# Optimization experiments

Hardware: AMD Instinct MI355X
Metric: run time of the kernel (lower is better)

The kernel has to match this reference:

```python
import jax, jax.numpy as jnp
import numpy as np

N = 100000      # nodes
E = 1200000     # edges
F = 16          # in_cont_dim
EMB = 8         # emb_dim
H = 64          # hidden_dim
NL = 3          # num_layers
NT = 32         # num_func_types


def setup_inputs() -> dict:
    key = jax.random.key(0)
    ks = jax.random.split(key, 10)
    s = lambda k, sh: jax.random.normal(k, sh, jnp.float32) * 0.05
    inp = {}
    inp["x_cont"] = jax.random.normal(ks[0], (N, F), jnp.float32)
    inp["func_type"] = jax.random.randint(ks[1], (N,), 0, NT)
    inp["edge_index"] = jax.random.randint(ks[2], (2, E), 0, N)
    inp["emb_table"] = s(ks[3], (NT, EMB))
    inp["W_in"] = s(ks[4], (F + EMB, H)); inp["b_in"] = jnp.zeros((H,), jnp.float32)
    inp["W_g"] = s(ks[5], (NL, H, H));    inp["b_g"] = jnp.zeros((NL, H), jnp.float32)
    inp["W_o1"] = s(ks[6], (H, H));       inp["b_o1"] = jnp.zeros((H,), jnp.float32)
    inp["W_o2"] = s(ks[7], (H, 1));       inp["b_o2"] = jnp.zeros((1,), jnp.float32)
    return inp


def _gcn_layer(x, src, dst, deg_isq, W, b):
    # PyG GCNConv: h = x W; out_i = sum_{j->i} d_i^-1/2 d_j^-1/2 h_j + d_i^-1 h_i + b
    h = x @ W                                   # [N, H]
    norm = deg_isq[src] * deg_isq[dst]          # [E]
    agg = jax.ops.segment_sum(norm[:, None] * h[src], dst, num_segments=N)
    agg = agg + (deg_isq * deg_isq)[:, None] * h  # self-loop contribution
    return agg + b


def reference(x_cont, func_type, edge_index, emb_table, W_in, b_in,
              W_g, b_g, W_o1, b_o1, W_o2, b_o2):
    src, dst = edge_index[0], edge_index[1]
    # degree with self loops (weight 1), computed at target nodes as in gcn_norm
    deg = 1.0 + jax.ops.segment_sum(jnp.ones((E,), x_cont.dtype), dst, num_segments=N)
    deg_isq = jax.lax.rsqrt(deg)
    x = jnp.concatenate([x_cont, emb_table[func_type]], axis=-1)  # [N, F+EMB]
    x = jax.nn.relu(x @ W_in + b_in)
    for i in range(NL):
        x = jax.nn.relu(_gcn_layer(x, src, dst, deg_isq, W_g[i], b_g[i]))
        # dropout is identity in eval mode
    h = jax.nn.relu(x @ W_o1 + b_o1)
    return (h @ W_o2 + b_o2)[:, 0]  # [N]
```

## Files before the change

kernel.cpp:

```cpp
#include <hip/hip_runtime.h>

#define HD 64
#define FC 16
#define FEMB 8

__global__ void k_count_rank(const int* __restrict__ dst, int* __restrict__ cnt,
                             int* __restrict__ rank, int E) {
    int e = blockIdx.x * blockDim.x + threadIdx.x;
    if (e >= E) return;
    rank[e] = atomicAdd(&cnt[dst[e]], 1);
}

__global__ void k_scan1(const int* __restrict__ cnt, int* __restrict__ row_part,
                        int* __restrict__ bsum, float* __restrict__ disq, int n) {
    __shared__ int s[256];
    int t = threadIdx.x;
    int i = blockIdx.x * 256 + t;
    int v = (i < n) ? cnt[i] : 0;
    if (i < n) disq[i] = rsqrtf(1.0f + (float)v);
    s[t] = v;
    __syncthreads();
    for (int off = 1; off < 256; off <<= 1) {
        int a = (t >= off) ? s[t - off] : 0;
        __syncthreads();
        s[t] += a;
        __syncthreads();
    }
    if (i < n) row_part[i] = s[t] - v;
    if (t == 255) bsum[blockIdx.x] = s[255];
}

__global__ void k_scan2(int* __restrict__ bsum, int nb) {
    __shared__ int s[1024];
    int t = threadIdx.x;
    int v = (t < nb) ? bsum[t] : 0;
    s[t] = v;
    __syncthreads();
    for (int off = 1; off < 1024; off <<= 1) {
        int a = (t >= off) ? s[t - off] : 0;
        __syncthreads();
        s[t] += a;
        __syncthreads();
    }
    if (t < nb) bsum[t] = s[t] - v;
}

__global__ void k_scan3(int* __restrict__ row_part, const int* __restrict__ bsum, int n) {
    int stride = gridDim.x * blockDim.x;
    for (int i = blockIdx.x * blockDim.x + threadIdx.x; i < n; i += stride)
        row_part[i] += bsum[i >> 8];
}

__global__ void k_reorder(const int* __restrict__ src, const int* __restrict__ dst,
                          const int* __restrict__ rank, const int* __restrict__ rowst,
                          int* __restrict__ csr, int E) {
    int e = blockIdx.x * blockDim.x + threadIdx.x;
    if (e >= E) return;
    csr[rowst[dst[e]] + rank[e]] = src[e];
}

__global__ void k_input(const float* __restrict__ xc, const int* __restrict__ ft,
                        const float* __restrict__ emb, const float* __restrict__ Win,
                        const float* __restrict__ bin, const float* __restrict__ disq,
                        float* __restrict__ y, int n) {
    int lane = threadIdx.x & 63;
    int wid  = (blockIdx.x * blockDim.x + threadIdx.x) >> 6;
    if (wid >= n) return;
    float acc = bin[lane];
    const float* xr = xc + (size_t)wid * FC;
#pragma unroll
    for (int k = 0; k < FC; k++)
        acc = fmaf(xr[k], Win[k * HD + lane], acc);
    int t = ft[wid];
    const float* er = emb + (size_t)t * FEMB;
#pragma unroll
    for (int k = 0; k < FEMB; k++)
        acc = fmaf(er[k], Win[(FC + k) * HD + lane], acc);
    y[(size_t)wid * HD + lane] = fmaxf(acc, 0.0f) * disq[wid];
}

__global__ void k_agg(const float4* __restrict__ y4, const int* __restrict__ csr,
                      const int* __restrict__ rs, const int* __restrict__ deg,
                      const float* __restrict__ disq, float4* __restrict__ agg4, int n) {
    int lane = threadIdx.x & 63;
    int node = (blockIdx.x * blockDim.x + threadIdx.x) >> 6;
    if (node >= n) return;
    int g  = lane >> 4;
    int c4 = lane & 15;
    int start = rs[node];
    int end   = start + deg[node];
    float4 acc = {0, 0, 0, 0};
    for (int j = start; j < end; j += 16) {
#pragma unroll
        for (int slot = 0; slot < 4; slot++) {
            int e = j + slot * 4 + g;
            bool ok = e < end;
            int ec = ok ? e : j;
            int s = csr[ec];
            float4 v = y4[(size_t)s * 16 + c4];
            if (ok) {
                acc.x += v.x; acc.y += v.y; acc.z += v.z; acc.w += v.w;
            }
        }
    }
    acc.x += __shfl_xor(acc.x, 16); acc.y += __shfl_xor(acc.y, 16);
    acc.z += __shfl_xor(acc.z, 16); acc.w += __shfl_xor(acc.w, 16);
    acc.x += __shfl_xor(acc.x, 32); acc.y += __shfl_xor(acc.y, 32);
    acc.z += __shfl_xor(acc.z, 32); acc.w += __shfl_xor(acc.w, 32);
    if (g == 0) {
        float4 self = y4[(size_t)node * 16 + c4];
        float di = disq[node];
        float4 o;
        o.x = di * (acc.x + self.x);
        o.y = di * (acc.y + self.y);
        o.z = di * (acc.z + self.z);
        o.w = di * (acc.w + self.w);
        agg4[(size_t)node * 16 + c4] = o;
    }
}

__global__ __launch_bounds__(256, 4)
void k_mm(float* __restrict__ x, const float* __restrict__ W,
          const float* __restrict__ b, const float* __restrict__ disq, int n) {
    __shared__ float4 ws4[64][16];
    __shared__ float4 xs4[64][17];
    int tid = threadIdx.x;
    int node0 = blockIdx.x * 64;

    for (int i = tid; i < 1024; i += 256)
        ws4[i >> 4][i & 15] = ((const float4*)W)[i];
    for (int i = tid; i < 1024; i += 256) {
        int nn = i >> 4, k4 = i & 15;
        int row = node0 + nn; if (row >= n) row = n - 1;
        xs4[nn][k4] = ((const float4*)(x + (size_t)row * HD))[k4];
    }
    __syncthreads();

    int tc4 = tid & 15;
    int tn  = (tid >> 4) * 4;
    float4 ac0 = {0,0,0,0}, ac1 = {0,0,0,0}, ac2 = {0,0,0,0}, ac3 = {0,0,0,0};

#pragma unroll 4
    for (int k4 = 0; k4 < 16; k4++) {
        float4 w0 = ws4[k4 * 4 + 0][tc4];
        float4 w1 = ws4[k4 * 4 + 1][tc4];
        float4 w2 = ws4[k4 * 4 + 2][tc4];
        float4 w3 = ws4[k4 * 4 + 3][tc4];
#pragma unroll
        for (int i = 0; i < 4; i++) {
            float4 xv = xs4[tn + i][k4];
            float4* ac = (i == 0) ? &ac0 : (i == 1) ? &ac1 : (i == 2) ? &ac2 : &ac3;
            ac->x = fmaf(xv.x, w0.x, ac->x); ac->y = fmaf(xv.x, w0.y, ac->y);
            ac->z = fmaf(xv.x, w0.z, ac->z); ac->w = fmaf(xv.x, w0.w, ac->w);
            ac->x = fmaf(xv.y, w1.x, ac->x); ac->y = fmaf(xv.y, w1.y, ac->y);
            ac->z = fmaf(xv.y, w1.z, ac->z); ac->w = fmaf(xv.y, w1.w, ac->w);
            ac->x = fmaf(xv.z, w2.x, ac->x); ac->y = fmaf(xv.z, w2.y, ac->y);
            ac->z = fmaf(xv.z, w2.z, ac->z); ac->w = fmaf(xv.z, w2.w, ac->w);
            ac->x = fmaf(xv.w, w3.x, ac->x); ac->y = fmaf(xv.w, w3.y, ac->y);
            ac->z = fmaf(xv.w, w3.z, ac->z); ac->w = fmaf(xv.w, w3.w, ac->w);
        }
    }

    float4 bb = ((const float4*)b)[tc4];
    float4 accs[4] = {ac0, ac1, ac2, ac3};
#pragma unroll
    for (int i = 0; i < 4; i++) {
        int row = node0 + tn + i;
        if (row < n) {
            float dq = disq[row];
            float4 o;
            o.x = fmaxf(accs[i].x + bb.x, 0.0f) * dq;
            o.y = fmaxf(accs[i].y + bb.y, 0.0f) * dq;
            o.z = fmaxf(accs[i].z + bb.z, 0.0f) * dq;
            o.w = fmaxf(accs[i].w + bb.w, 0.0f) * dq;
            *(float4*)(x + (size_t)row * HD + tc4 * 4) = o;
        }
    }
}

__global__ __launch_bounds__(256, 4)
void k_mm_head(const float* __restrict__ x, const float* __restrict__ W,
               const float* __restrict__ b, const float* __restrict__ W1,
               const float* __restrict__ b1, const float* __restrict__ W2,
               const float* __restrict__ b2, float* __restrict__ out, int n) {
    __shared__ float4 ws4[64][16];
    __shared__ float4 xs4[64][17];
    int tid = threadIdx.x;
    int node0 = blockIdx.x * 64;

    for (int i = tid; i < 1024; i += 256)
        ws4[i >> 4][i & 15] = ((const float4*)W)[i];
    for (int i = tid; i < 1024; i += 256) {
        int nn = i >> 4, k4 = i & 15;
        int row = node0 + nn; if (row >= n) row = n - 1;
        xs4[nn][k4] = ((const float4*)(x + (size_t)row * HD))[k4];
    }
    __syncthreads();

    int tc4 = tid & 15;
    int tn  = (tid >> 4) * 4;

    float4 ac0 = {0,0,0,0}, ac1 = {0,0,0,0}, ac2 = {0,0,0,0}, ac3 = {0,0,0,0};
#pragma unroll 4
    for (int k4 = 0; k4 < 16; k4++) {
        float4 w0 = ws4[k4 * 4 + 0][tc4];
        float4 w1 = ws4[k4 * 4 + 1][tc4];
        float4 w2 = ws4[k4 * 4 + 2][tc4];
        float4 w3 = ws4[k4 * 4 + 3][tc4];
#pragma unroll
        for (int i = 0; i < 4; i++) {
            float4 xv = xs4[tn + i][k4];
            float4* ac = (i == 0) ? &ac0 : (i == 1) ? &ac1 : (i == 2) ? &ac2 : &ac3;
            ac->x = fmaf(xv.x, w0.x, ac->x); ac->y = fmaf(xv.x, w0.y, ac->y);
            ac->z = fmaf(xv.x, w0.z, ac->z); ac->w = fmaf(xv.x, w0.w, ac->w);
            ac->x = fmaf(xv.y, w1.x, ac->x); ac->y = fmaf(xv.y, w1.y, ac->y);
            ac->z = fmaf(xv.y, w1.z, ac->z); ac->w = fmaf(xv.y, w1.w, ac->w);
            ac->x = fmaf(xv.z, w2.x, ac->x); ac->y = fmaf(xv.z, w2.y, ac->y);
            ac->z = fmaf(xv.z, w2.z, ac->z); ac->w = fmaf(xv.z, w2.w, ac->w);
            ac->x = fmaf(xv.w, w3.x, ac->x); ac->y = fmaf(xv.w, w3.y, ac->y);
            ac->z = fmaf(xv.w, w3.z, ac->z); ac->w = fmaf(xv.w, w3.w, ac->w);
        }
    }
    __syncthreads();

    {
        float4 bb = ((const float4*)b)[tc4];
        float4 accs[4] = {ac0, ac1, ac2, ac3};
#pragma unroll
        for (int i = 0; i < 4; i++) {
            float4 o;
            o.x = fmaxf(accs[i].x + bb.x, 0.0f);
            o.y = fmaxf(accs[i].y + bb.y, 0.0f);
            o.z = fmaxf(accs[i].z + bb.z, 0.0f);
            o.w = fmaxf(accs[i].w + bb.w, 0.0f);
            xs4[tn + i][tc4] = o;
        }
    }
    for (int i = tid; i < 1024; i += 256)
        ws4[i >> 4][i & 15] = ((const float4*)W1)[i];
    __syncthreads();

    float4 bc0 = {0,0,0,0}, bc1 = {0,0,0,0}, bc2 = {0,0,0,0}, bc3 = {0,0,0,0};
#pragma unroll 4
    for (int k4 = 0; k4 < 16; k4++) {
        float4 w0 = ws4[k4 * 4 + 0][tc4];
        float4 w1 = ws4[k4 * 4 + 1][tc4];
        float4 w2 = ws4[k4 * 4 + 2][tc4];
        float4 w3 = ws4[k4 * 4 + 3][tc4];
#pragma unroll
        for (int i = 0; i < 4; i++) {
            float4 xv = xs4[tn + i][k4];
            float4* ac = (i == 0) ? &bc0 : (i == 1) ? &bc1 : (i == 2) ? &bc2 : &bc3;
            ac->x = fmaf(xv.x, w0.x, ac->x); ac->y = fmaf(xv.x, w0.y, ac->y);
            ac->z = fmaf(xv.x, w0.z, ac->z); ac->w = fmaf(xv.x, w0.w, ac->w);
            ac->x = fmaf(xv.y, w1.x, ac->x); ac->y = fmaf(xv.y, w1.y, ac->y);
            ac->z = fmaf(xv.y, w1.z, ac->z); ac->w = fmaf(xv.y, w1.w, ac->w);
            ac->x = fmaf(xv.z, w2.x, ac->x); ac->y = fmaf(xv.z, w2.y, ac->y);
            ac->z = fmaf(xv.z, w2.z, ac->z); ac->w = fmaf(xv.z, w2.w, ac->w);
            ac->x = fmaf(xv.w, w3.x, ac->x); ac->y = fmaf(xv.w, w3.y, ac->y);
            ac->z = fmaf(xv.w, w3.z, ac->z); ac->w = fmaf(xv.w, w3.w, ac->w);
        }
    }

    float4 b1v = ((const float4*)b1)[tc4];
    float4 w2v = ((const float4*)W2)[tc4];
    float b2v  = b2[0];
    float4 bcs[4] = {bc0, bc1, bc2, bc3};
#pragma unroll
    for (int i = 0; i < 4; i++) {
        float s = fmaxf(bcs[i].x + b1v.x, 0.0f) * w2v.x
                + fmaxf(bcs[i].y + b1v.y, 0.0f) * w2v.y
                + fmaxf(bcs[i].z + b1v.z, 0.0f) * w2v.z
                + fmaxf(bcs[i].w + b1v.w, 0.0f) * w2v.w;
        s += __shfl_xor(s, 1);
        s += __shfl_xor(s, 2);
        s += __shfl_xor(s, 4);
        s += __shfl_xor(s, 8);
        int row = node0 + tn + i;
        if (tc4 == 0 && row < n) out[row] = s + b2v;
    }
}

extern "C" void kernel_launch(void* const* d_in, const int* in_sizes, int n_in,
                              void* d_out, int out_size, void* d_ws, size_t ws_size,
                              hipStream_t stream) {
    const float* x_cont = (const float*)d_in[0];
    const int*   ftyp   = (const int*)d_in[1];
    const int*   eidx   = (const int*)d_in[2];
    const float* emb    = (const float*)d_in[3];
    const float* W_in   = (const float*)d_in[4];
    const float* b_in   = (const float*)d_in[5];
    const float* W_g    = (const float*)d_in[6];
    const float* b_g    = (const float*)d_in[7];
    const float* W_o1   = (const float*)d_in[8];
    const float* b_o1   = (const float*)d_in[9];
    const float* W_o2   = (const float*)d_in[10];
    const float* b_o2   = (const float*)d_in[11];
    float* out = (float*)d_out;

    const int n = in_sizes[1];
    const int E = in_sizes[2] / 2;
    const int* src = eidx;
    const int* dst = eidx + E;

    char* p = (char*)d_ws;
    auto alloc = [&](size_t bytes) {
        char* r = p;
        p += (bytes + 255) & ~(size_t)255;
        return r;
    };
    int*   cnt   = (int*)  alloc((size_t)n * 4);
    float* disq  = (float*)alloc((size_t)n * 4);
    int*   rowst = (int*)  alloc((size_t)n * 4);
    int*   bsum  = (int*)  alloc(4096);
    int*   rank  = (int*)  alloc((size_t)E * 4);
    int*   csr   = (int*)  alloc((size_t)E * 4);
    float* xb    = (float*)alloc((size_t)n * HD * 4);
    float* xo    = (float*)alloc((size_t)n * HD * 4);

    hipMemsetAsync(cnt, 0, (size_t)n * 4, stream);

    dim3 blk(256);
    const int nb1   = (n + 255) / 256;
    const int nb_e  = (E + 255) / 256;
    const int nb_nw = (n + 3) / 4;
    const int nb_t  = (n + 63) / 64;

    k_count_rank<<<nb_e, blk, 0, stream>>>(dst, cnt, rank, E);
    k_scan1<<<nb1, blk, 0, stream>>>(cnt, rowst, bsum, disq, n);
    k_scan2<<<1, 1024, 0, stream>>>(bsum, nb1);
    k_scan3<<<512, blk, 0, stream>>>(rowst, bsum, n);
    k_reorder<<<nb_e, blk, 0, stream>>>(src, dst, rank, rowst, csr, E);
    k_input<<<nb_nw, blk, 0, stream>>>(x_cont, ftyp, emb, W_in, b_in, disq, xb, n);

    float* a = xb;
    float* bpp = xo;
    for (int L = 0; L < 2; L++) {
        k_agg<<<nb_nw, blk, 0, stream>>>((const float4*)a, csr, rowst, cnt, disq,
                                         (float4*)bpp, n);
        k_mm<<<nb_t, blk, 0, stream>>>(bpp, W_g + (size_t)L * HD * HD,
                                       b_g + (size_t)L * HD, disq, n);
        float* t = a; a = bpp; bpp = t;
    }
    k_agg<<<nb_nw, blk, 0, stream>>>((const float4*)a, csr, rowst, cnt, disq,
                                     (float4*)bpp, n);
    k_mm_head<<<nb_t, blk, 0, stream>>>(bpp, W_g + (size_t)2 * HD * HD,
                                        b_g + (size_t)2 * HD,
                                        W_o1, b_o1, W_o2, b_o2, out, n);
}
```

Measured before the change: 367.5 us.

## Fuse neighbor aggregation into per-layer matmul kernel via shared memory

Each GCN layer's gather-aggregation is merged into the 64-node-tile matmul kernel. Each wavefront aggregates 16 nodes sequentially and writes the results into the shared-memory x tile, and the tile is then multiplied by W. This removes the intermediate aggregation buffer write/read and three kernel launches. The cost is far fewer concurrent wavefronts on the gather, since each wave now handles 16 nodes serially instead of one node per wave, which may cut memory-level parallelism for the random gathers.

```diff
diff --git a/kernel.cpp b/kernel.cpp
--- a/kernel.cpp
+++ b/kernel.cpp
@@ -79,67 +79,70 @@
     y[(size_t)wid * HD + lane] = fmaxf(acc, 0.0f) * disq[wid];
 }
 
-__global__ void k_agg(const float4* __restrict__ y4, const int* __restrict__ csr,
-                      const int* __restrict__ rs, const int* __restrict__ deg,
-                      const float* __restrict__ disq, float4* __restrict__ agg4, int n) {
-    int lane = threadIdx.x & 63;
-    int node = (blockIdx.x * blockDim.x + threadIdx.x) >> 6;
-    if (node >= n) return;
-    int g  = lane >> 4;
-    int c4 = lane & 15;
-    int start = rs[node];
-    int end   = start + deg[node];
-    float4 acc = {0, 0, 0, 0};
-    for (int j = start; j < end; j += 16) {
-#pragma unroll
-        for (int slot = 0; slot < 4; slot++) {
-            int e = j + slot * 4 + g;
-            bool ok = e < end;
-            int ec = ok ? e : j;
-            int s = csr[ec];
-            float4 v = y4[(size_t)s * 16 + c4];
-            if (ok) {
-                acc.x += v.x; acc.y += v.y; acc.z += v.z; acc.w += v.w;
+
+__device__ __forceinline__
+void agg_phase(const float4* __restrict__ y4, const int* __restrict__ csr,
+               const int* __restrict__ rowst, const int* __restrict__ cnt,
+               const float* __restrict__ disq, float4 (*xs4)[17],
+               int node0, int n, int tid) {
+    int lane = tid & 63;
+    int w    = tid >> 6;
+    int g    = lane >> 4;
+    int c4   = lane & 15;
+    int base = node0 + w * 16;
+
+    int hidx = base + (lane & 15);
+    int hcl  = hidx < n ? hidx : n - 1;
+    int   rsv  = rowst[hcl];
+    int   cntv = cnt[hcl];
+    float dqv  = disq[hcl];
+
+    for (int nn = 0; nn < 16; nn++) {
+        int node = base + nn;
+        bool valid = node < n;
+        int   start = __shfl(rsv, nn);
+        int   deg   = __shfl(cntv, nn);
+        float di    = __shfl(dqv, nn);
+        float4 acc = {0, 0, 0, 0};
+        if (valid) {
+            int end = start + deg;
+            for (int j = start; j < end; j += 16) {
+#pragma unroll
+                for (int slot = 0; slot < 4; slot++) {
+                    int e = j + slot * 4 + g;
+                    bool ok = e < end;
+                    int ec = ok ? e : j;
+                    int s = csr[ec];
+                    float4 v = y4[(size_t)s * 16 + c4];
+                    if (ok) {
+                        acc.x += v.x; acc.y += v.y; acc.z += v.z; acc.w += v.w;
+                    }
+                }
             }
         }
-    }
-    acc.x += __shfl_xor(acc.x, 16); acc.y += __shfl_xor(acc.y, 16);
-    acc.z += __shfl_xor(acc.z, 16); acc.w += __shfl_xor(acc.w, 16);
-    acc.x += __shfl_xor(acc.x, 32); acc.y += __shfl_xor(acc.y, 32);
-    acc.z += __shfl_xor(acc.z, 32); acc.w += __shfl_xor(acc.w, 32);
-    if (g == 0) {
-        float4 self = y4[(size_t)node * 16 + c4];
-        float di = disq[node];
-        float4 o;
-        o.x = di * (acc.x + self.x);
-        o.y = di * (acc.y + self.y);
-        o.z = di * (acc.z + self.z);
-        o.w = di * (acc.w + self.w);
-        agg4[(size_t)node * 16 + c4] = o;
-    }
-}
-
-__global__ __launch_bounds__(256, 4)
-void k_mm(float* __restrict__ x, const float* __restrict__ W,
-          const float* __restrict__ b, const float* __restrict__ disq, int n) {
-    __shared__ float4 ws4[64][16];
-    __shared__ float4 xs4[64][17];
-    int tid = threadIdx.x;
-    int node0 = blockIdx.x * 64;
-
-    for (int i = tid; i < 1024; i += 256)
-        ws4[i >> 4][i & 15] = ((const float4*)W)[i];
-    for (int i = tid; i < 1024; i += 256) {
-        int nn = i >> 4, k4 = i & 15;
-        int row = node0 + nn; if (row >= n) row = n - 1;
-        xs4[nn][k4] = ((const float4*)(x + (size_t)row * HD))[k4];
-    }
-    __syncthreads();
-
+        acc.x += __shfl_xor(acc.x, 16); acc.y += __shfl_xor(acc.y, 16);
+        acc.z += __shfl_xor(acc.z, 16); acc.w += __shfl_xor(acc.w, 16);
+        acc.x += __shfl_xor(acc.x, 32); acc.y += __shfl_xor(acc.y, 32);
+        acc.z += __shfl_xor(acc.z, 32); acc.w += __shfl_xor(acc.w, 32);
+        if (g == 0) {
+            float4 o = {0, 0, 0, 0};
+            if (valid) {
+                float4 self = y4[(size_t)node * 16 + c4];
+                o.x = di * (acc.x + self.x);
+                o.y = di * (acc.y + self.y);
+                o.z = di * (acc.z + self.z);
+                o.w = di * (acc.w + self.w);
+            }
+            xs4[w * 16 + nn][c4] = o;
+        }
+    }
+}
+
+__device__ __forceinline__
+void mm_phase(const float4 (*ws4)[16], const float4 (*xs4)[17], int tid,
+              float4* ac0, float4* ac1, float4* ac2, float4* ac3) {
     int tc4 = tid & 15;
     int tn  = (tid >> 4) * 4;
-    float4 ac0 = {0,0,0,0}, ac1 = {0,0,0,0}, ac2 = {0,0,0,0}, ac3 = {0,0,0,0};
-
 #pragma unroll 4
     for (int k4 = 0; k4 < 16; k4++) {
         float4 w0 = ws4[k4 * 4 + 0][tc4];
@@ -149,7 +152,7 @@
 #pragma unroll
         for (int i = 0; i < 4; i++) {
             float4 xv = xs4[tn + i][k4];
-            float4* ac = (i == 0) ? &ac0 : (i == 1) ? &ac1 : (i == 2) ? &ac2 : &ac3;
+            float4* ac = (i == 0) ? ac0 : (i == 1) ? ac1 : (i == 2) ? ac2 : ac3;
             ac->x = fmaf(xv.x, w0.x, ac->x); ac->y = fmaf(xv.x, w0.y, ac->y);
             ac->z = fmaf(xv.x, w0.z, ac->z); ac->w = fmaf(xv.x, w0.w, ac->w);
             ac->x = fmaf(xv.y, w1.x, ac->x); ac->y = fmaf(xv.y, w1.y, ac->y);
@@ -160,7 +163,29 @@
             ac->z = fmaf(xv.w, w3.z, ac->z); ac->w = fmaf(xv.w, w3.w, ac->w);
         }
     }
-
+}
+
+__global__ __launch_bounds__(256, 4)
+void k_layer_mm(const float4* __restrict__ y4, const int* __restrict__ csr,
+                const int* __restrict__ rowst, const int* __restrict__ cnt,
+                const float* __restrict__ disq, const float* __restrict__ W,
+                const float* __restrict__ b, float* __restrict__ yo, int n) {
+    __shared__ float4 ws4[64][16];
+    __shared__ float4 xs4[64][17];
+    int tid = threadIdx.x;
+    int node0 = blockIdx.x * 64;
+
+    for (int i = tid; i < 1024; i += 256)
+        ws4[i >> 4][i & 15] = ((const float4*)W)[i];
+
+    agg_phase(y4, csr, rowst, cnt, disq, xs4, node0, n, tid);
+    __syncthreads();
+
+    float4 ac0 = {0,0,0,0}, ac1 = {0,0,0,0}, ac2 = {0,0,0,0}, ac3 = {0,0,0,0};
+    mm_phase(ws4, xs4, tid, &ac0, &ac1, &ac2, &ac3);
+
+    int tc4 = tid & 15;
+    int tn  = (tid >> 4) * 4;
     float4 bb = ((const float4*)b)[tc4];
     float4 accs[4] = {ac0, ac1, ac2, ac3};
 #pragma unroll
@@ -173,16 +198,18 @@
             o.y = fmaxf(accs[i].y + bb.y, 0.0f) * dq;
             o.z = fmaxf(accs[i].z + bb.z, 0.0f) * dq;
             o.w = fmaxf(accs[i].w + bb.w, 0.0f) * dq;
-            *(float4*)(x + (size_t)row * HD + tc4 * 4) = o;
+            *(float4*)(yo + (size_t)row * HD + tc4 * 4) = o;
         }
     }
 }
 
 __global__ __launch_bounds__(256, 4)
-void k_mm_head(const float* __restrict__ x, const float* __restrict__ W,
-               const float* __restrict__ b, const float* __restrict__ W1,
-               const float* __restrict__ b1, const float* __restrict__ W2,
-               const float* __restrict__ b2, float* __restrict__ out, int n) {
+void k_layer_head(const float4* __restrict__ y4, const int* __restrict__ csr,
+                  const int* __restrict__ rowst, const int* __restrict__ cnt,
+                  const float* __restrict__ disq, const float* __restrict__ W,
+                  const float* __restrict__ b, const float* __restrict__ W1,
+                  const float* __restrict__ b1, const float* __restrict__ W2,
+                  const float* __restrict__ b2, float* __restrict__ out, int n) {
     __shared__ float4 ws4[64][16];
     __shared__ float4 xs4[64][17];
     int tid = threadIdx.x;
@@ -190,39 +217,16 @@
 
     for (int i = tid; i < 1024; i += 256)
         ws4[i >> 4][i & 15] = ((const float4*)W)[i];
-    for (int i = tid; i < 1024; i += 256) {
-        int nn = i >> 4, k4 = i & 15;
-        int row = node0 + nn; if (row >= n) row = n - 1;
-        xs4[nn][k4] = ((const float4*)(x + (size_t)row * HD))[k4];
-    }
+
+    agg_phase(y4, csr, rowst, cnt, disq, xs4, node0, n, tid);
+    __syncthreads();
+
+    float4 ac0 = {0,0,0,0}, ac1 = {0,0,0,0}, ac2 = {0,0,0,0}, ac3 = {0,0,0,0};
+    mm_phase(ws4, xs4, tid, &ac0, &ac1, &ac2, &ac3);
     __syncthreads();
 
     int tc4 = tid & 15;
     int tn  = (tid >> 4) * 4;
-
-    float4 ac0 = {0,0,0,0}, ac1 = {0,0,0,0}, ac2 = {0,0,0,0}, ac3 = {0,0,0,0};
-#pragma unroll 4
-    for (int k4 = 0; k4 < 16; k4++) {
-        float4 w0 = ws4[k4 * 4 + 0][tc4];
-        float4 w1 = ws4[k4 * 4 + 1][tc4];
-        float4 w2 = ws4[k4 * 4 + 2][tc4];
-        float4 w3 = ws4[k4 * 4 + 3][tc4];
-#pragma unroll
-        for (int i = 0; i < 4; i++) {
-            float4 xv = xs4[tn + i][k4];
-            float4* ac = (i == 0) ? &ac0 : (i == 1) ? &ac1 : (i == 2) ? &ac2 : &ac3;
-            ac->x = fmaf(xv.x, w0.x, ac->x); ac->y = fmaf(xv.x, w0.y, ac->y);
-            ac->z = fmaf(xv.x, w0.z, ac->z); ac->w = fmaf(xv.x, w0.w, ac->w);
-            ac->x = fmaf(xv.y, w1.x, ac->x); ac->y = fmaf(xv.y, w1.y, ac->y);
-            ac->z = fmaf(xv.y, w1.z, ac->z); ac->w = fmaf(xv.y, w1.w, ac->w);
-            ac->x = fmaf(xv.z, w2.x, ac->x); ac->y = fmaf(xv.z, w2.y, ac->y);
-            ac->z = fmaf(xv.z, w2.z, ac->z); ac->w = fmaf(xv.z, w2.w, ac->w);
-            ac->x = fmaf(xv.w, w3.x, ac->x); ac->y = fmaf(xv.w, w3.y, ac->y);
-            ac->z = fmaf(xv.w, w3.z, ac->z); ac->w = fmaf(xv.w, w3.w, ac->w);
-        }
-    }
-    __syncthreads();
-
     {
         float4 bb = ((const float4*)b)[tc4];
         float4 accs[4] = {ac0, ac1, ac2, ac3};
@@ -241,26 +245,7 @@
     __syncthreads();
 
     float4 bc0 = {0,0,0,0}, bc1 = {0,0,0,0}, bc2 = {0,0,0,0}, bc3 = {0,0,0,0};
-#pragma unroll 4
-    for (int k4 = 0; k4 < 16; k4++) {
-        float4 w0 = ws4[k4 * 4 + 0][tc4];
-        float4 w1 = ws4[k4 * 4 + 1][tc4];
-        float4 w2 = ws4[k4 * 4 + 2][tc4];
-        float4 w3 = ws4[k4 * 4 + 3][tc4];
-#pragma unroll
-        for (int i = 0; i < 4; i++) {
-            float4 xv = xs4[tn + i][k4];
-            float4* ac = (i == 0) ? &bc0 : (i == 1) ? &bc1 : (i == 2) ? &bc2 : &bc3;
-            ac->x = fmaf(xv.x, w0.x, ac->x); ac->y = fmaf(xv.x, w0.y, ac->y);
-            ac->z = fmaf(xv.x, w0.z, ac->z); ac->w = fmaf(xv.x, w0.w, ac->w);
-            ac->x = fmaf(xv.y, w1.x, ac->x); ac->y = fmaf(xv.y, w1.y, ac->y);
-            ac->z = fmaf(xv.y, w1.z, ac->z); ac->w = fmaf(xv.y, w1.w, ac->w);
-            ac->x = fmaf(xv.z, w2.x, ac->x); ac->y = fmaf(xv.z, w2.y, ac->y);
-            ac->z = fmaf(xv.z, w2.z, ac->z); ac->w = fmaf(xv.z, w2.w, ac->w);
-            ac->x = fmaf(xv.w, w3.x, ac->x); ac->y = fmaf(xv.w, w3.y, ac->y);
-            ac->z = fmaf(xv.w, w3.z, ac->z); ac->w = fmaf(xv.w, w3.w, ac->w);
-        }
-    }
+    mm_phase(ws4, xs4, tid, &bc0, &bc1, &bc2, &bc3);
 
     float4 b1v = ((const float4*)b1)[tc4];
     float4 w2v = ((const float4*)W2)[tc4];
@@ -333,18 +318,11 @@
     k_reorder<<<nb_e, blk, 0, stream>>>(src, dst, rank, rowst, csr, E);
     k_input<<<nb_nw, blk, 0, stream>>>(x_cont, ftyp, emb, W_in, b_in, disq, xb, n);
 
-    float* a = xb;
-    float* bpp = xo;
-    for (int L = 0; L < 2; L++) {
-        k_agg<<<nb_nw, blk, 0, stream>>>((const float4*)a, csr, rowst, cnt, disq,
-                                         (float4*)bpp, n);
-        k_mm<<<nb_t, blk, 0, stream>>>(bpp, W_g + (size_t)L * HD * HD,
-                                       b_g + (size_t)L * HD, disq, n);
-        float* t = a; a = bpp; bpp = t;
-    }
-    k_agg<<<nb_nw, blk, 0, stream>>>((const float4*)a, csr, rowst, cnt, disq,
-                                     (float4*)bpp, n);
-    k_mm_head<<<nb_t, blk, 0, stream>>>(bpp, W_g + (size_t)2 * HD * HD,
-                                        b_g + (size_t)2 * HD,
-                                        W_o1, b_o1, W_o2, b_o2, out, n);
-}
+    k_layer_mm<<<nb_t, blk, 0, stream>>>((const float4*)xb, csr, rowst, cnt, disq,
+                                         W_g + 0 * HD * HD, b_g + 0 * HD, xo, n);
+    k_layer_mm<<<nb_t, blk, 0, stream>>>((const float4*)xo, csr, rowst, cnt, disq,
+                                         W_g + 1 * HD * HD, b_g + 1 * HD, xb, n);
+    k_layer_head<<<nb_t, blk, 0, stream>>>((const float4*)xb, csr, rowst, cnt, disq,
+                                           W_g + 2 * HD * HD, b_g + 2 * HD,
+                                           W_o1, b_o1, W_o2, b_o2, out, n);
+}
```

Result: slower. 444.0 us (+20.8%).
